# Performance work log

Hardware: AMD Instinct MI355X
Metric: run time of the kernel (lower is better)

Reference implementation:

```python
import jax, jax.numpy as jnp
import numpy as np

N_NODES = 100000
N_EDGES = 1600000
IN_FEATS = 256
OUT_FEATS = 64


def setup_inputs() -> dict:
    key = jax.random.key(0)
    k1, k2, k3, k4, k5, k6 = jax.random.split(key, 6)
    x = jax.random.normal(k1, (N_NODES, IN_FEATS), dtype=jnp.float32)
    edge_src = jax.random.randint(k2, (N_EDGES,), 0, N_NODES, dtype=jnp.int32)
    edge_dst = jax.random.randint(k3, (N_EDGES,), 0, N_NODES, dtype=jnp.int32)
    edge_weight = jax.random.uniform(k4, (N_EDGES,), dtype=jnp.float32)
    # Linear(in_feats, out_feats) params (Kaiming-uniform-ish init scale)
    scale = 1.0 / np.sqrt(IN_FEATS)
    W = jax.random.uniform(k5, (IN_FEATS, OUT_FEATS), minval=-scale, maxval=scale, dtype=jnp.float32)
    b = jax.random.uniform(k6, (OUT_FEATS,), minval=-scale, maxval=scale, dtype=jnp.float32)
    return {"x": x, "edge_src": edge_src, "edge_dst": edge_dst,
            "edge_weight": edge_weight, "W": W, "b": b}


def reference(x, edge_src, edge_dst, edge_weight, W, b):
    # h = fc(x)
    h = x @ W + b                                   # [N, out_feats]
    # spmm(graph, h): out[dst] += w * h[src]  (weighted adjacency matvec)
    msgs = h[edge_src] * edge_weight[:, None]       # [E, out_feats]
    out = jax.ops.segment_sum(msgs, edge_dst, num_segments=N_NODES)
    return out
```

## Files before the change

kernel.cpp:

```cpp
#include <hip/hip_runtime.h>

#define IN_F 256
#define OUT_F 64
#define SORT_CHUNK 4096
#define BKT_SHIFT 7
#define BKT_NODES 128
#define MAX_NB 1024

typedef __attribute__((ext_vector_type(8))) short short8;
typedef __attribute__((ext_vector_type(4))) float f32x4;

static __device__ __forceinline__ short f2bf(float f) {
    union { float f; unsigned u; } v; v.f = f;
    unsigned r = v.u + 0x7FFFu + ((v.u >> 16) & 1u);
    return (short)(r >> 16);
}
static __device__ __forceinline__ float bf2f(short s) {
    return __int_as_float(((unsigned)(unsigned short)s) << 16);
}

__global__ __launch_bounds__(256)
void prep_w_kernel(const float* __restrict__ W, short* __restrict__ Wt) {
    int i = blockIdx.x * 256 + threadIdx.x;
    if (i < IN_F * OUT_F) {
        int k = i / OUT_F, n = i % OUT_F;
        Wt[n * IN_F + k] = f2bf(W[i]);
    }
}

__global__ __launch_bounds__(256, 4)
void fc_bhist_kernel(const float* __restrict__ x, const short* __restrict__ Wt,
                     const float* __restrict__ bias, short* __restrict__ h,
                     const int* __restrict__ dst, int* __restrict__ counts,
                     int nRows, int nE, int NB, int nSB, int nHist) {
    __shared__ __align__(16) char smem[OUT_F * IN_F * sizeof(short)];
    if ((int)blockIdx.x < nHist) {
        int* lh = (int*)smem;
        const int cb = blockIdx.x;
        for (int b0 = threadIdx.x; b0 < NB; b0 += 256) lh[b0] = 0;
        __syncthreads();
        const int base = cb * SORT_CHUNK;
        const int lim = min(nE, base + SORT_CHUNK);
        const int4* d4 = (const int4*)(dst + base);
        const int n4 = (lim - base) >> 2;
        for (int i = threadIdx.x; i < n4; i += 256) {
            int4 v = d4[i];
            atomicAdd(&lh[v.x >> BKT_SHIFT], 1);
            atomicAdd(&lh[v.y >> BKT_SHIFT], 1);
            atomicAdd(&lh[v.z >> BKT_SHIFT], 1);
            atomicAdd(&lh[v.w >> BKT_SHIFT], 1);
        }
        for (int e = base + (n4 << 2) + threadIdx.x; e < lim; e += 256)
            atomicAdd(&lh[dst[e] >> BKT_SHIFT], 1);
        __syncthreads();
        for (int b0 = threadIdx.x; b0 < NB; b0 += 256)
            counts[b0 * nSB + cb] = lh[b0];
        return;
    }
    short* Wl = (short*)smem;
    {
        const uint4* src = (const uint4*)Wt;
        #pragma unroll
        for (int it = 0; it < 8; ++it) {
            int g = it * 256 + threadIdx.x;
            int n = g >> 5, s = g & 31;
            *(uint4*)((char*)Wl + n * 512 + (s ^ (n & 7)) * 16) = src[g];
        }
    }
    __syncthreads();

    const int wv = threadIdx.x >> 6;
    const int l  = threadIdx.x & 63;
    const int lr = l & 15;
    const int kg = l >> 4;

    const int fb = blockIdx.x - nHist;
    const int rowbase = (fb * 4 + wv) * 32;
    if (rowbase >= nRows) return;

    const int ar0 = min(rowbase + lr,      nRows - 1);
    const int ar1 = min(rowbase + 16 + lr, nRows - 1);
    const float* xp0 = x + (size_t)ar0 * IN_F + kg * 8;
    const float* xp1 = x + (size_t)ar1 * IN_F + kg * 8;

    f32x4 acc[2][4];
    #pragma unroll
    for (int m = 0; m < 2; ++m)
        #pragma unroll
        for (int n = 0; n < 4; ++n) acc[m][n] = (f32x4)0.f;

    #pragma unroll
    for (int kt = 0; kt < 8; ++kt) {
        const int K0 = kt * 32;
        float4 a0lo = *(const float4*)(xp0 + K0);
        float4 a0hi = *(const float4*)(xp0 + K0 + 4);
        float4 a1lo = *(const float4*)(xp1 + K0);
        float4 a1hi = *(const float4*)(xp1 + K0 + 4);

        short8 a0, a1;
        a0[0] = f2bf(a0lo.x); a0[1] = f2bf(a0lo.y);
        a0[2] = f2bf(a0lo.z); a0[3] = f2bf(a0lo.w);
        a0[4] = f2bf(a0hi.x); a0[5] = f2bf(a0hi.y);
        a0[6] = f2bf(a0hi.z); a0[7] = f2bf(a0hi.w);
        a1[0] = f2bf(a1lo.x); a1[1] = f2bf(a1lo.y);
        a1[2] = f2bf(a1lo.z); a1[3] = f2bf(a1lo.w);
        a1[4] = f2bf(a1hi.x); a1[5] = f2bf(a1hi.y);
        a1[6] = f2bf(a1hi.z); a1[7] = f2bf(a1hi.w);

        short8 bf[4];
        #pragma unroll
        for (int nt = 0; nt < 4; ++nt) {
            const int col = nt * 16 + lr;
            const int slot = (kt * 4 + kg) ^ (col & 7);
            bf[nt] = *(const short8*)((const char*)Wl + col * 512 + slot * 16);
        }
        #pragma unroll
        for (int nt = 0; nt < 4; ++nt) {
            acc[0][nt] = __builtin_amdgcn_mfma_f32_16x16x32_bf16(a0, bf[nt], acc[0][nt], 0, 0, 0);
            acc[1][nt] = __builtin_amdgcn_mfma_f32_16x16x32_bf16(a1, bf[nt], acc[1][nt], 0, 0, 0);
        }
    }

    #pragma unroll
    for (int m = 0; m < 2; ++m) {
        #pragma unroll
        for (int nt = 0; nt < 4; ++nt) {
            const int col = nt * 16 + lr;
            const float bb = bias[col];
            #pragma unroll
            for (int j = 0; j < 4; ++j) {
                const int r = rowbase + m * 16 + kg * 4 + j;
                if (r < nRows)
                    h[(size_t)r * OUT_F + col] = f2bf(acc[m][nt][j] + bb);
            }
        }
    }
}

__global__ __launch_bounds__(256)
void scan1_kernel(const int* __restrict__ cnt, int* __restrict__ off,
                  int* __restrict__ part, int n) {
    __shared__ int sh[256];
    int base = blockIdx.x * 1024;
    int t = threadIdx.x;
    int v[4]; int s = 0;
    #pragma unroll
    for (int i = 0; i < 4; ++i) {
        int idx = base + t * 4 + i;
        v[i] = (idx < n) ? cnt[idx] : 0;
        s += v[i];
    }
    sh[t] = s;
    __syncthreads();
    for (int d = 1; d < 256; d <<= 1) {
        int val = (t >= d) ? sh[t - d] : 0;
        __syncthreads();
        sh[t] += val;
        __syncthreads();
    }
    if (t == 255) part[blockIdx.x] = sh[255];
    int run = (t == 0) ? 0 : sh[t - 1];
    #pragma unroll
    for (int i = 0; i < 4; ++i) {
        int idx = base + t * 4 + i;
        if (idx < n) off[idx] = run;
        run += v[i];
    }
}

__global__ __launch_bounds__(256)
void scan2_kernel(int* __restrict__ part, int nPart) {
    __shared__ int sh[256];
    int t = threadIdx.x;
    int v[4]; int s = 0;
    #pragma unroll
    for (int i = 0; i < 4; ++i) {
        int idx = t * 4 + i;
        v[i] = (idx < nPart) ? part[idx] : 0;
        s += v[i];
    }
    sh[t] = s;
    __syncthreads();
    for (int d = 1; d < 256; d <<= 1) {
        int val = (t >= d) ? sh[t - d] : 0;
        __syncthreads();
        sh[t] += val;
        __syncthreads();
    }
    int run = (t == 0) ? 0 : sh[t - 1];
    #pragma unroll
    for (int i = 0; i < 4; ++i) {
        int idx = t * 4 + i;
        if (idx < nPart) part[idx] = run;
        run += v[i];
    }
}

__global__ __launch_bounds__(256)
void bfill_kernel(const int* __restrict__ src, const int* __restrict__ dst,
                  const float* __restrict__ w, const int* __restrict__ bases,
                  const int* __restrict__ part, int2* __restrict__ pack,
                  int nE, int NB, int nSB) {
    __shared__ int cur[MAX_NB];
    const int cb = blockIdx.x;
    for (int b0 = threadIdx.x; b0 < NB; b0 += 256) {
        int idx = b0 * nSB + cb;
        cur[b0] = bases[idx] + part[idx >> 10];
    }
    __syncthreads();
    const int base = cb * SORT_CHUNK;
    const int lim = min(nE, base + SORT_CHUNK);
    const int4* s4 = (const int4*)(src + base);
    const int4* d4 = (const int4*)(dst + base);
    const float4* w4 = (const float4*)(w + base);
    const int n4 = (lim - base) >> 2;
    for (int i = threadIdx.x; i < n4; i += 256) {
        int4 s = s4[i]; int4 d = d4[i]; float4 ww = w4[i];
        int p0 = atomicAdd(&cur[d.x >> BKT_SHIFT], 1);
        pack[p0] = make_int2(s.x | ((d.x & (BKT_NODES - 1)) << 17), __float_as_int(ww.x));
        int p1 = atomicAdd(&cur[d.y >> BKT_SHIFT], 1);
        pack[p1] = make_int2(s.y | ((d.y & (BKT_NODES - 1)) << 17), __float_as_int(ww.y));
        int p2 = atomicAdd(&cur[d.z >> BKT_SHIFT], 1);
        pack[p2] = make_int2(s.z | ((d.z & (BKT_NODES - 1)) << 17), __float_as_int(ww.z));
        int p3 = atomicAdd(&cur[d.w >> BKT_SHIFT], 1);
        pack[p3] = make_int2(s.w | ((d.w & (BKT_NODES - 1)) << 17), __float_as_int(ww.w));
    }
    for (int e = base + (n4 << 2) + threadIdx.x; e < lim; e += 256) {
        int d = dst[e];
        int p = atomicAdd(&cur[d >> BKT_SHIFT], 1);
        pack[p] = make_int2(src[e] | ((d & (BKT_NODES - 1)) << 17),
                            __float_as_int(w[e]));
    }
}

__global__ __launch_bounds__(256)
void nsort_kernel(const int2* __restrict__ pack, const int* __restrict__ bases,
                  const int* __restrict__ part, int2* __restrict__ pack2,
                  int* __restrict__ off, int nRows, int nE, int NB, int nSB) {
    __shared__ int cnt[BKT_NODES];
    __shared__ int scn[BKT_NODES];
    const int b = blockIdx.x;
    const int tid = threadIdx.x;
    const int i0 = b * nSB;
    const int segStart = bases[i0] + part[i0 >> 10];
    int segEnd = nE;
    if (b + 1 < NB) {
        int i1 = (b + 1) * nSB;
        segEnd = bases[i1] + part[i1 >> 10];
    }

    if (tid < BKT_NODES) cnt[tid] = 0;
    __syncthreads();
    {
        int e = segStart + tid;
        for (; e + 768 < segEnd; e += 1024) {
            int a0 = pack[e].x, a1 = pack[e + 256].x;
            int a2 = pack[e + 512].x, a3 = pack[e + 768].x;
            atomicAdd(&cnt[(a0 >> 17) & (BKT_NODES - 1)], 1);
            atomicAdd(&cnt[(a1 >> 17) & (BKT_NODES - 1)], 1);
            atomicAdd(&cnt[(a2 >> 17) & (BKT_NODES - 1)], 1);
            atomicAdd(&cnt[(a3 >> 17) & (BKT_NODES - 1)], 1);
        }
        for (; e < segEnd; e += 256)
            atomicAdd(&cnt[(pack[e].x >> 17) & (BKT_NODES - 1)], 1);
    }
    __syncthreads();

    if (tid < BKT_NODES) scn[tid] = cnt[tid];
    __syncthreads();
    for (int d = 1; d < BKT_NODES; d <<= 1) {
        int t = 0;
        if (tid < BKT_NODES && tid >= d) t = scn[tid - d];
        __syncthreads();
        if (tid < BKT_NODES) scn[tid] += t;
        __syncthreads();
    }

    const int node0 = b * BKT_NODES;
    const int ncnt = min(BKT_NODES, nRows - node0);
    if (tid < ncnt)
        off[node0 + tid] = segStart + scn[tid] - cnt[tid];
    if (tid == 0 && node0 + ncnt == nRows)
        off[nRows] = segEnd;
    __syncthreads();

    if (tid < BKT_NODES) cnt[tid] = segStart + scn[tid] - cnt[tid];
    __syncthreads();
    {
        int e = segStart + tid;
        for (; e + 768 < segEnd; e += 1024) {
            int2 p0 = pack[e], p1 = pack[e + 256];
            int2 p2 = pack[e + 512], p3 = pack[e + 768];
            int q0 = atomicAdd(&cnt[(p0.x >> 17) & (BKT_NODES - 1)], 1);
            pack2[q0] = make_int2(p0.x & 0x1FFFF, p0.y);
            int q1 = atomicAdd(&cnt[(p1.x >> 17) & (BKT_NODES - 1)], 1);
            pack2[q1] = make_int2(p1.x & 0x1FFFF, p1.y);
            int q2 = atomicAdd(&cnt[(p2.x >> 17) & (BKT_NODES - 1)], 1);
            pack2[q2] = make_int2(p2.x & 0x1FFFF, p2.y);
            int q3 = atomicAdd(&cnt[(p3.x >> 17) & (BKT_NODES - 1)], 1);
            pack2[q3] = make_int2(p3.x & 0x1FFFF, p3.y);
        }
        for (; e < segEnd; e += 256) {
            int2 p = pack[e];
            int q = atomicAdd(&cnt[(p.x >> 17) & (BKT_NODES - 1)], 1);
            pack2[q] = make_int2(p.x & 0x1FFFF, p.y);
        }
    }
}

__global__ __launch_bounds__(256)
void ngather_kernel(const short* __restrict__ h, const int* __restrict__ off,
                    const int2* __restrict__ pack2, float* __restrict__ out,
                    int nNodes) {
    int wid = (blockIdx.x * 256 + threadIdx.x) >> 6;
    int lane = threadIdx.x & 63;
    if (wid >= nNodes) return;
    int e = off[wid], end = off[wid + 1];
    const ushort* hu = (const ushort*)h;
    float acc = 0.f;
    for (; e + 8 <= end; e += 8) {
        int2 pk[8];
        #pragma unroll
        for (int i = 0; i < 8; ++i) pk[i] = pack2[e + i];
        float hv[8];
        #pragma unroll
        for (int i = 0; i < 8; ++i)
            hv[i] = bf2f((short)hu[(size_t)pk[i].x * OUT_F + lane]);
        #pragma unroll
        for (int i = 0; i < 8; ++i)
            acc = fmaf(__int_as_float(pk[i].y), hv[i], acc);
    }
    for (; e + 4 <= end; e += 4) {
        int2 pk[4];
        #pragma unroll
        for (int i = 0; i < 4; ++i) pk[i] = pack2[e + i];
        #pragma unroll
        for (int i = 0; i < 4; ++i)
            acc = fmaf(__int_as_float(pk[i].y),
                       bf2f((short)hu[(size_t)pk[i].x * OUT_F + lane]), acc);
    }
    for (; e < end; ++e) {
        int2 p = pack2[e];
        acc = fmaf(__int_as_float(p.y),
                   bf2f((short)hu[(size_t)p.x * OUT_F + lane]), acc);
    }
    out[(size_t)wid * OUT_F + lane] = acc;
}

__global__ __launch_bounds__(256)
void scatter_kernel(const short* __restrict__ h, const int* __restrict__ src,
                    const int* __restrict__ dst, const float* __restrict__ w,
                    float* __restrict__ out, int nE) {
    int t = blockIdx.x * 256 + threadIdx.x;
    int c = t & 15;
    int stride = (gridDim.x * 256) >> 4;
    for (int e = t >> 4; e < nE; e += stride) {
        int s = src[e];
        int d = dst[e];
        float ww = w[e];
        float* op = out + (size_t)d * OUT_F + c * 4;
        const short* hp = h + (size_t)s * OUT_F + c * 4;
        unsafeAtomicAdd(op + 0, ww * bf2f(hp[0]));
        unsafeAtomicAdd(op + 1, ww * bf2f(hp[1]));
        unsafeAtomicAdd(op + 2, ww * bf2f(hp[2]));
        unsafeAtomicAdd(op + 3, ww * bf2f(hp[3]));
    }
}

static inline size_t align256(size_t x) { return (x + 255) & ~(size_t)255; }

extern "C" void kernel_launch(void* const* d_in, const int* in_sizes, int n_in,
                              void* d_out, int out_size, void* d_ws, size_t ws_size,
                              hipStream_t stream) {
    const float* x    = (const float*)d_in[0];
    const int*   esrc = (const int*)d_in[1];
    const int*   edst = (const int*)d_in[2];
    const float* ew   = (const float*)d_in[3];
    const float* W    = (const float*)d_in[4];
    const float* b    = (const float*)d_in[5];

    int nRows = in_sizes[0] / IN_F;
    int nE    = in_sizes[1];

    int NB  = (nRows + BKT_NODES - 1) / BKT_NODES;
    int nSB = (nE + SORT_CHUNK - 1) / SORT_CHUNK;
    int nCnt = NB * nSB;
    int nPart = (nCnt + 1023) / 1024;

    char* p = (char*)d_ws;
    size_t hB    = align256((size_t)nRows * OUT_F * sizeof(short));
    size_t wtB   = align256((size_t)IN_F * OUT_F * sizeof(short));
    size_t cntB  = align256((size_t)nCnt * sizeof(int));
    size_t basB  = align256((size_t)nCnt * sizeof(int));
    size_t partB = align256((size_t)nPart * sizeof(int));
    size_t packB = align256((size_t)nE * sizeof(int2));
    size_t offB  = align256((size_t)(nRows + 1) * sizeof(int));
    size_t need  = hB + wtB + cntB + basB + partB + 2 * packB + offB;

    short* h      = (short*)p;  p += hB;
    short* Wt     = (short*)p;  p += wtB;
    int*   counts = (int*)p;    p += cntB;
    int*   bases  = (int*)p;    p += basB;
    int*   part   = (int*)p;    p += partB;
    int2*  pack   = (int2*)p;   p += packB;
    int2*  pack2  = (int2*)p;   p += packB;
    int*   off    = (int*)p;

    float* out = (float*)d_out;

    bool ok = (ws_size >= need) && (NB <= MAX_NB) && (nPart <= 1024) &&
              (nRows < (1 << 17));
    int nHist = ok ? nSB : 0;
    int fcBlocks = (nRows + 127) / 128;

    prep_w_kernel<<<(IN_F * OUT_F + 255) / 256, 256, 0, stream>>>(W, Wt);
    fc_bhist_kernel<<<nHist + fcBlocks, 256, 0, stream>>>(
        x, Wt, b, h, edst, counts, nRows, nE, NB, nSB, nHist);

    if (ok) {
        scan1_kernel<<<nPart, 256, 0, stream>>>(counts, bases, part, nCnt);
        scan2_kernel<<<1, 256, 0, stream>>>(part, nPart);
        bfill_kernel<<<nSB, 256, 0, stream>>>(esrc, edst, ew, bases, part,
                                              pack, nE, NB, nSB);
        nsort_kernel<<<NB, 256, 0, stream>>>(pack, bases, part, pack2, off,
                                             nRows, nE, NB, nSB);
        int gBlocks = (nRows * 64 + 255) / 256;
        ngather_kernel<<<gBlocks, 256, 0, stream>>>(h, off, pack2, out, nRows);
    } else {
        hipMemsetAsync(out, 0, (size_t)out_size * sizeof(float), stream);
        scatter_kernel<<<4096, 256, 0, stream>>>(h, esrc, edst, ew, out, nE);
    }
}
```

Measured before the change: 286.4 us.

## Fuse FC, bucket sort and gather into one cooperative persistent kernel

Replaces the chain of separate launches (weight prep, fc+histogram, two scans, bucket fill, node sort, gather) with a single cooperative kernel. The phases are separated by grid.sync and run in persistent grid-stride loops. Weight bf16 conversion and swizzling now happen inside each block instead of in a separate prep kernel. This removes launch gaps and tail effects between phases. In exchange the grid is capped at occupancy-limited size (at most 1024 blocks), which may reduce parallelism in the gather and GEMM phases, and it adds grid-wide barrier costs plus host-side occupancy queries on every call.

```diff
diff --git a/kernel.cpp b/kernel.cpp
--- a/kernel.cpp
+++ b/kernel.cpp
@@ -1,4 +1,7 @@
 #include <hip/hip_runtime.h>
+#include <hip/hip_cooperative_groups.h>
+
+namespace cg = cooperative_groups;
 
 #define IN_F 256
 #define OUT_F 64
@@ -6,6 +9,7 @@
 #define BKT_SHIFT 7
 #define BKT_NODES 128
 #define MAX_NB 1024
+#define GRID_MAX 1024
 
 typedef __attribute__((ext_vector_type(8))) short short8;
 typedef __attribute__((ext_vector_type(4))) float f32x4;
@@ -19,67 +23,35 @@
     return __int_as_float(((unsigned)(unsigned short)s) << 16);
 }
 
-__global__ __launch_bounds__(256)
-void prep_w_kernel(const float* __restrict__ W, short* __restrict__ Wt) {
-    int i = blockIdx.x * 256 + threadIdx.x;
-    if (i < IN_F * OUT_F) {
-        int k = i / OUT_F, n = i % OUT_F;
-        Wt[n * IN_F + k] = f2bf(W[i]);
-    }
-}
-
-__global__ __launch_bounds__(256, 4)
-void fc_bhist_kernel(const float* __restrict__ x, const short* __restrict__ Wt,
-                     const float* __restrict__ bias, short* __restrict__ h,
-                     const int* __restrict__ dst, int* __restrict__ counts,
-                     int nRows, int nE, int NB, int nSB, int nHist) {
-    __shared__ __align__(16) char smem[OUT_F * IN_F * sizeof(short)];
-    if ((int)blockIdx.x < nHist) {
-        int* lh = (int*)smem;
-        const int cb = blockIdx.x;
-        for (int b0 = threadIdx.x; b0 < NB; b0 += 256) lh[b0] = 0;
-        __syncthreads();
-        const int base = cb * SORT_CHUNK;
-        const int lim = min(nE, base + SORT_CHUNK);
-        const int4* d4 = (const int4*)(dst + base);
-        const int n4 = (lim - base) >> 2;
-        for (int i = threadIdx.x; i < n4; i += 256) {
-            int4 v = d4[i];
-            atomicAdd(&lh[v.x >> BKT_SHIFT], 1);
-            atomicAdd(&lh[v.y >> BKT_SHIFT], 1);
-            atomicAdd(&lh[v.z >> BKT_SHIFT], 1);
-            atomicAdd(&lh[v.w >> BKT_SHIFT], 1);
-        }
-        for (int e = base + (n4 << 2) + threadIdx.x; e < lim; e += 256)
-            atomicAdd(&lh[dst[e] >> BKT_SHIFT], 1);
-        __syncthreads();
-        for (int b0 = threadIdx.x; b0 < NB; b0 += 256)
-            counts[b0 * nSB + cb] = lh[b0];
-        return;
-    }
-    short* Wl = (short*)smem;
-    {
-        const uint4* src = (const uint4*)Wt;
-        #pragma unroll
-        for (int it = 0; it < 8; ++it) {
-            int g = it * 256 + threadIdx.x;
-            int n = g >> 5, s = g & 31;
-            *(uint4*)((char*)Wl + n * 512 + (s ^ (n & 7)) * 16) = src[g];
-        }
-    }
-    __syncthreads();
-
-    const int wv = threadIdx.x >> 6;
-    const int l  = threadIdx.x & 63;
+
+static __device__ __forceinline__ void stage_W(const float* __restrict__ W,
+                                               short* Wl, int tid) {
+    const int n0 = tid & 63;
+    const int kb = tid >> 6;
+    #pragma unroll
+    for (int K0 = 0; K0 < 64; K0 += 8) {
+        const int k0 = kb * 64 + K0;
+        short8 v;
+        #pragma unroll
+        for (int j = 0; j < 8; ++j)
+            v[j] = f2bf(W[(k0 + j) * OUT_F + n0]);
+        *(short8*)((char*)Wl + n0 * 512 + (((k0 >> 3)) ^ (n0 & 7)) * 16) = v;
+    }
+}
+
+static __device__ __forceinline__ void gemm_tile(const float* __restrict__ x,
+                                                 const short* Wl,
+                                                 const float* __restrict__ bias,
+                                                 short* __restrict__ h,
+                                                 int rowbase, int nRows, int tid) {
+    const int wv = tid >> 6;
+    const int l  = tid & 63;
     const int lr = l & 15;
     const int kg = l >> 4;
-
-    const int fb = blockIdx.x - nHist;
-    const int rowbase = (fb * 4 + wv) * 32;
-    if (rowbase >= nRows) return;
-
-    const int ar0 = min(rowbase + lr,      nRows - 1);
-    const int ar1 = min(rowbase + 16 + lr, nRows - 1);
+    const int rb = rowbase + wv * 32;
+    if (rb >= nRows) return;
+    const int ar0 = min(rb + lr,      nRows - 1);
+    const int ar1 = min(rb + 16 + lr, nRows - 1);
     const float* xp0 = x + (size_t)ar0 * IN_F + kg * 8;
     const float* xp1 = x + (size_t)ar1 * IN_F + kg * 8;
 
@@ -129,7 +101,7 @@
             const float bb = bias[col];
             #pragma unroll
             for (int j = 0; j < 4; ++j) {
-                const int r = rowbase + m * 16 + kg * 4 + j;
+                const int r = rb + m * 16 + kg * 4 + j;
                 if (r < nRows)
                     h[(size_t)r * OUT_F + col] = f2bf(acc[m][nt][j] + bb);
             }
@@ -137,73 +109,37 @@
     }
 }
 
-__global__ __launch_bounds__(256)
-void scan1_kernel(const int* __restrict__ cnt, int* __restrict__ off,
-                  int* __restrict__ part, int n) {
-    __shared__ int sh[256];
-    int base = blockIdx.x * 1024;
-    int t = threadIdx.x;
-    int v[4]; int s = 0;
-    #pragma unroll
-    for (int i = 0; i < 4; ++i) {
-        int idx = base + t * 4 + i;
-        v[i] = (idx < n) ? cnt[idx] : 0;
-        s += v[i];
-    }
-    sh[t] = s;
-    __syncthreads();
-    for (int d = 1; d < 256; d <<= 1) {
-        int val = (t >= d) ? sh[t - d] : 0;
-        __syncthreads();
-        sh[t] += val;
-        __syncthreads();
-    }
-    if (t == 255) part[blockIdx.x] = sh[255];
-    int run = (t == 0) ? 0 : sh[t - 1];
-    #pragma unroll
-    for (int i = 0; i < 4; ++i) {
-        int idx = base + t * 4 + i;
-        if (idx < n) off[idx] = run;
-        run += v[i];
-    }
-}
-
-__global__ __launch_bounds__(256)
-void scan2_kernel(int* __restrict__ part, int nPart) {
-    __shared__ int sh[256];
-    int t = threadIdx.x;
-    int v[4]; int s = 0;
-    #pragma unroll
-    for (int i = 0; i < 4; ++i) {
-        int idx = t * 4 + i;
-        v[i] = (idx < nPart) ? part[idx] : 0;
-        s += v[i];
-    }
-    sh[t] = s;
-    __syncthreads();
-    for (int d = 1; d < 256; d <<= 1) {
-        int val = (t >= d) ? sh[t - d] : 0;
-        __syncthreads();
-        sh[t] += val;
-        __syncthreads();
-    }
-    int run = (t == 0) ? 0 : sh[t - 1];
-    #pragma unroll
-    for (int i = 0; i < 4; ++i) {
-        int idx = t * 4 + i;
-        if (idx < nPart) part[idx] = run;
-        run += v[i];
-    }
-}
-
-__global__ __launch_bounds__(256)
-void bfill_kernel(const int* __restrict__ src, const int* __restrict__ dst,
-                  const float* __restrict__ w, const int* __restrict__ bases,
-                  const int* __restrict__ part, int2* __restrict__ pack,
-                  int nE, int NB, int nSB) {
-    __shared__ int cur[MAX_NB];
-    const int cb = blockIdx.x;
-    for (int b0 = threadIdx.x; b0 < NB; b0 += 256) {
+static __device__ __forceinline__ void hist_chunk(const int* __restrict__ dst,
+                                                  int* lh, int* __restrict__ counts,
+                                                  int cb, int nE, int NB, int nSB,
+                                                  int tid) {
+    for (int b0 = tid; b0 < NB; b0 += 256) lh[b0] = 0;
+    __syncthreads();
+    const int base = cb * SORT_CHUNK;
+    const int lim = min(nE, base + SORT_CHUNK);
+    const int4* d4 = (const int4*)(dst + base);
+    const int n4 = (lim - base) >> 2;
+    for (int i = tid; i < n4; i += 256) {
+        int4 v = d4[i];
+        atomicAdd(&lh[v.x >> BKT_SHIFT], 1);
+        atomicAdd(&lh[v.y >> BKT_SHIFT], 1);
+        atomicAdd(&lh[v.z >> BKT_SHIFT], 1);
+        atomicAdd(&lh[v.w >> BKT_SHIFT], 1);
+    }
+    for (int e = base + (n4 << 2) + tid; e < lim; e += 256)
+        atomicAdd(&lh[dst[e] >> BKT_SHIFT], 1);
+    __syncthreads();
+    for (int b0 = tid; b0 < NB; b0 += 256)
+        counts[b0 * nSB + cb] = lh[b0];
+    __syncthreads();
+}
+
+static __device__ __forceinline__ void bfill_chunk(
+        const int* __restrict__ src, const int* __restrict__ dst,
+        const float* __restrict__ w, const int* __restrict__ bases,
+        const int* __restrict__ part, int2* __restrict__ pack,
+        int* cur, int cb, int nE, int NB, int nSB, int tid) {
+    for (int b0 = tid; b0 < NB; b0 += 256) {
         int idx = b0 * nSB + cb;
         cur[b0] = bases[idx] + part[idx >> 10];
     }
@@ -214,7 +150,7 @@
     const int4* d4 = (const int4*)(dst + base);
     const float4* w4 = (const float4*)(w + base);
     const int n4 = (lim - base) >> 2;
-    for (int i = threadIdx.x; i < n4; i += 256) {
+    for (int i = tid; i < n4; i += 256) {
         int4 s = s4[i]; int4 d = d4[i]; float4 ww = w4[i];
         int p0 = atomicAdd(&cur[d.x >> BKT_SHIFT], 1);
         pack[p0] = make_int2(s.x | ((d.x & (BKT_NODES - 1)) << 17), __float_as_int(ww.x));
@@ -225,22 +161,20 @@
         int p3 = atomicAdd(&cur[d.w >> BKT_SHIFT], 1);
         pack[p3] = make_int2(s.w | ((d.w & (BKT_NODES - 1)) << 17), __float_as_int(ww.w));
     }
-    for (int e = base + (n4 << 2) + threadIdx.x; e < lim; e += 256) {
+    for (int e = base + (n4 << 2) + tid; e < lim; e += 256) {
         int d = dst[e];
         int p = atomicAdd(&cur[d >> BKT_SHIFT], 1);
         pack[p] = make_int2(src[e] | ((d & (BKT_NODES - 1)) << 17),
                             __float_as_int(w[e]));
     }
-}
-
-__global__ __launch_bounds__(256)
-void nsort_kernel(const int2* __restrict__ pack, const int* __restrict__ bases,
-                  const int* __restrict__ part, int2* __restrict__ pack2,
-                  int* __restrict__ off, int nRows, int nE, int NB, int nSB) {
-    __shared__ int cnt[BKT_NODES];
-    __shared__ int scn[BKT_NODES];
-    const int b = blockIdx.x;
-    const int tid = threadIdx.x;
+    __syncthreads();
+}
+
+static __device__ __forceinline__ void nsort_bucket(
+        const int2* __restrict__ pack, const int* __restrict__ bases,
+        const int* __restrict__ part, int2* __restrict__ pack2,
+        int* __restrict__ off, int* cnt, int* scn,
+        int b, int nRows, int nE, int NB, int nSB, int tid) {
     const int i0 = b * nSB;
     const int segStart = bases[i0] + part[i0 >> 10];
     int segEnd = nE;
@@ -248,7 +182,6 @@
         int i1 = (b + 1) * nSB;
         segEnd = bases[i1] + part[i1 >> 10];
     }
-
     if (tid < BKT_NODES) cnt[tid] = 0;
     __syncthreads();
     {
@@ -265,7 +198,6 @@
             atomicAdd(&cnt[(pack[e].x >> 17) & (BKT_NODES - 1)], 1);
     }
     __syncthreads();
-
     if (tid < BKT_NODES) scn[tid] = cnt[tid];
     __syncthreads();
     for (int d = 1; d < BKT_NODES; d <<= 1) {
@@ -275,7 +207,6 @@
         if (tid < BKT_NODES) scn[tid] += t;
         __syncthreads();
     }
-
     const int node0 = b * BKT_NODES;
     const int ncnt = min(BKT_NODES, nRows - node0);
     if (tid < ncnt)
@@ -283,7 +214,6 @@
     if (tid == 0 && node0 + ncnt == nRows)
         off[nRows] = segEnd;
     __syncthreads();
-
     if (tid < BKT_NODES) cnt[tid] = segStart + scn[tid] - cnt[tid];
     __syncthreads();
     {
@@ -306,6 +236,248 @@
             pack2[q] = make_int2(p.x & 0x1FFFF, p.y);
         }
     }
+    __syncthreads();
+}
+
+static __device__ __forceinline__ float gather_node(
+        const ushort* __restrict__ hu, const int2* __restrict__ pack2,
+        int e, int end, int lane) {
+    float acc = 0.f;
+    for (; e + 8 <= end; e += 8) {
+        int2 pk[8];
+        #pragma unroll
+        for (int i = 0; i < 8; ++i) pk[i] = pack2[e + i];
+        float hv[8];
+        #pragma unroll
+        for (int i = 0; i < 8; ++i)
+            hv[i] = bf2f((short)hu[(size_t)pk[i].x * OUT_F + lane]);
+        #pragma unroll
+        for (int i = 0; i < 8; ++i)
+            acc = fmaf(__int_as_float(pk[i].y), hv[i], acc);
+    }
+    for (; e + 4 <= end; e += 4) {
+        int2 pk[4];
+        #pragma unroll
+        for (int i = 0; i < 4; ++i) pk[i] = pack2[e + i];
+        #pragma unroll
+        for (int i = 0; i < 4; ++i)
+            acc = fmaf(__int_as_float(pk[i].y),
+                       bf2f((short)hu[(size_t)pk[i].x * OUT_F + lane]), acc);
+    }
+    for (; e < end; ++e) {
+        int2 p = pack2[e];
+        acc = fmaf(__int_as_float(p.y),
+                   bf2f((short)hu[(size_t)p.x * OUT_F + lane]), acc);
+    }
+    return acc;
+}
+
+__global__ __launch_bounds__(256, 4)
+void mega_kernel(const float* __restrict__ x, const int* __restrict__ esrc,
+                 const int* __restrict__ edst, const float* __restrict__ ew,
+                 const float* __restrict__ W, const float* __restrict__ bias,
+                 short* __restrict__ h, int* __restrict__ counts,
+                 int* __restrict__ bases, int* __restrict__ part,
+                 int2* __restrict__ pack, int2* __restrict__ pack2,
+                 int* __restrict__ off, float* __restrict__ out,
+                 int nRows, int nE, int NB, int nSB, int nCnt, int nPart) {
+    cg::grid_group grid = cg::this_grid();
+    __shared__ __align__(16) char smem[32768];
+    const int tid = threadIdx.x;
+    const int bid = blockIdx.x;
+    const int nBlk = gridDim.x;
+
+    for (int cb = bid; cb < nSB; cb += nBlk)
+        hist_chunk(edst, (int*)smem, counts, cb, nE, NB, nSB, tid);
+
+    {
+        const int nTiles = (nRows + 127) / 128;
+        if (bid < nTiles) {
+            short* Wl = (short*)smem;
+            stage_W(W, Wl, tid);
+            __syncthreads();
+            for (int t = bid; t < nTiles; t += nBlk)
+                gemm_tile(x, Wl, bias, h, t * 128, nRows, tid);
+        }
+    }
+    grid.sync();
+
+    {
+        int* sh = (int*)smem;
+        for (int s = bid; s < nPart; s += nBlk) {
+            const int base = s * 1024;
+            int v[4]; int sum = 0;
+            #pragma unroll
+            for (int i = 0; i < 4; ++i) {
+                int idx = base + tid * 4 + i;
+                v[i] = (idx < nCnt) ? counts[idx] : 0;
+                sum += v[i];
+            }
+            sh[tid] = sum;
+            __syncthreads();
+            for (int d = 1; d < 256; d <<= 1) {
+                int val = (tid >= d) ? sh[tid - d] : 0;
+                __syncthreads();
+                sh[tid] += val;
+                __syncthreads();
+            }
+            if (tid == 255) part[s] = sh[255];
+            int run = (tid == 0) ? 0 : sh[tid - 1];
+            #pragma unroll
+            for (int i = 0; i < 4; ++i) {
+                int idx = base + tid * 4 + i;
+                if (idx < nCnt) bases[idx] = run;
+                run += v[i];
+            }
+            __syncthreads();
+        }
+    }
+    grid.sync();
+
+    if (bid == 0) {
+        int* sh = (int*)smem;
+        int v[4]; int sum = 0;
+        #pragma unroll
+        for (int i = 0; i < 4; ++i) {
+            int idx = tid * 4 + i;
+            v[i] = (idx < nPart) ? part[idx] : 0;
+            sum += v[i];
+        }
+        sh[tid] = sum;
+        __syncthreads();
+        for (int d = 1; d < 256; d <<= 1) {
+            int val = (tid >= d) ? sh[tid - d] : 0;
+            __syncthreads();
+            sh[tid] += val;
+            __syncthreads();
+        }
+        int run = (tid == 0) ? 0 : sh[tid - 1];
+        #pragma unroll
+        for (int i = 0; i < 4; ++i) {
+            int idx = tid * 4 + i;
+            if (idx < nPart) part[idx] = run;
+            run += v[i];
+        }
+    }
+    grid.sync();
+
+    for (int cb = bid; cb < nSB; cb += nBlk)
+        bfill_chunk(esrc, edst, ew, bases, part, pack, (int*)smem,
+                    cb, nE, NB, nSB, tid);
+    grid.sync();
+
+    {
+        int* cnt = (int*)smem;
+        int* scn = cnt + BKT_NODES;
+        for (int b = bid; b < NB; b += nBlk)
+            nsort_bucket(pack, bases, part, pack2, off, cnt, scn,
+                         b, nRows, nE, NB, nSB, tid);
+    }
+    grid.sync();
+
+    {
+        const int lane = tid & 63;
+        const int nW = (nBlk * 256) >> 6;
+        const ushort* hu = (const ushort*)h;
+        for (int wid = (bid * 256 + tid) >> 6; wid < nRows; wid += nW)
+            out[(size_t)wid * OUT_F + lane] =
+                gather_node(hu, pack2, off[wid], off[wid + 1], lane);
+    }
+}
+
+__global__ __launch_bounds__(256, 4)
+void fc_bhist_kernel(const float* __restrict__ x, const float* __restrict__ W,
+                     const float* __restrict__ bias, short* __restrict__ h,
+                     const int* __restrict__ dst, int* __restrict__ counts,
+                     int nRows, int nE, int NB, int nSB, int nHist) {
+    __shared__ __align__(16) char smem[32768];
+    if ((int)blockIdx.x < nHist) {
+        hist_chunk(dst, (int*)smem, counts, blockIdx.x, nE, NB, nSB, threadIdx.x);
+        return;
+    }
+    short* Wl = (short*)smem;
+    stage_W(W, Wl, threadIdx.x);
+    __syncthreads();
+    gemm_tile(x, Wl, bias, h, (blockIdx.x - nHist) * 128, nRows, threadIdx.x);
+}
+
+__global__ __launch_bounds__(256)
+void scan1_kernel(const int* __restrict__ cnt, int* __restrict__ off,
+                  int* __restrict__ part, int n) {
+    __shared__ int sh[256];
+    int base = blockIdx.x * 1024;
+    int t = threadIdx.x;
+    int v[4]; int s = 0;
+    #pragma unroll
+    for (int i = 0; i < 4; ++i) {
+        int idx = base + t * 4 + i;
+        v[i] = (idx < n) ? cnt[idx] : 0;
+        s += v[i];
+    }
+    sh[t] = s;
+    __syncthreads();
+    for (int d = 1; d < 256; d <<= 1) {
+        int val = (t >= d) ? sh[t - d] : 0;
+        __syncthreads();
+        sh[t] += val;
+        __syncthreads();
+    }
+    if (t == 255) part[blockIdx.x] = sh[255];
+    int run = (t == 0) ? 0 : sh[t - 1];
+    #pragma unroll
+    for (int i = 0; i < 4; ++i) {
+        int idx = base + t * 4 + i;
+        if (idx < n) off[idx] = run;
+        run += v[i];
+    }
+}
+
+__global__ __launch_bounds__(256)
+void scan2_kernel(int* __restrict__ part, int nPart) {
+    __shared__ int sh[256];
+    int t = threadIdx.x;
+    int v[4]; int s = 0;
+    #pragma unroll
+    for (int i = 0; i < 4; ++i) {
+        int idx = t * 4 + i;
+        v[i] = (idx < nPart) ? part[idx] : 0;
+        s += v[i];
+    }
+    sh[t] = s;
+    __syncthreads();
+    for (int d = 1; d < 256; d <<= 1) {
+        int val = (t >= d) ? sh[t - d] : 0;
+        __syncthreads();
+        sh[t] += val;
+        __syncthreads();
+    }
+    int run = (t == 0) ? 0 : sh[t - 1];
+    #pragma unroll
+    for (int i = 0; i < 4; ++i) {
+        int idx = t * 4 + i;
+        if (idx < nPart) part[idx] = run;
+        run += v[i];
+    }
+}
+
+__global__ __launch_bounds__(256)
+void bfill_kernel(const int* __restrict__ src, const int* __restrict__ dst,
+                  const float* __restrict__ w, const int* __restrict__ bases,
+                  const int* __restrict__ part, int2* __restrict__ pack,
+                  int nE, int NB, int nSB) {
+    __shared__ int cur[MAX_NB];
+    bfill_chunk(src, dst, w, bases, part, pack, cur,
+                blockIdx.x, nE, NB, nSB, threadIdx.x);
+}
+
+__global__ __launch_bounds__(256)
+void nsort_kernel(const int2* __restrict__ pack, const int* __restrict__ bases,
+                  const int* __restrict__ part, int2* __restrict__ pack2,
+                  int* __restrict__ off, int nRows, int nE, int NB, int nSB) {
+    __shared__ int cnt[BKT_NODES];
+    __shared__ int scn[BKT_NODES];
+    nsort_bucket(pack, bases, part, pack2, off, cnt, scn,
+                 blockIdx.x, nRows, nE, NB, nSB, threadIdx.x);
 }
 
 __global__ __launch_bounds__(256)
@@ -315,36 +487,8 @@
     int wid = (blockIdx.x * 256 + threadIdx.x) >> 6;
     int lane = threadIdx.x & 63;
     if (wid >= nNodes) return;
-    int e = off[wid], end = off[wid + 1];
-    const ushort* hu = (const ushort*)h;
-    float acc = 0.f;
-    for (; e + 8 <= end; e += 8) {
-        int2 pk[8];
-        #pragma unroll
-        for (int i = 0; i < 8; ++i) pk[i] = pack2[e + i];
-        float hv[8];
-        #pragma unroll
-        for (int i = 0; i < 8; ++i)
-            hv[i] = bf2f((short)hu[(size_t)pk[i].x * OUT_F + lane]);
-        #pragma unroll
-        for (int i = 0; i < 8; ++i)
-            acc = fmaf(__int_as_float(pk[i].y), hv[i], acc);
-    }
-    for (; e + 4 <= end; e += 4) {
-        int2 pk[4];
-        #pragma unroll
-        for (int i = 0; i < 4; ++i) pk[i] = pack2[e + i];
-        #pragma unroll
-        for (int i = 0; i < 4; ++i)
-            acc = fmaf(__int_as_float(pk[i].y),
-                       bf2f((short)hu[(size_t)pk[i].x * OUT_F + lane]), acc);
-    }
-    for (; e < end; ++e) {
-        int2 p = pack2[e];
-        acc = fmaf(__int_as_float(p.y),
-                   bf2f((short)hu[(size_t)p.x * OUT_F + lane]), acc);
-    }
-    out[(size_t)wid * OUT_F + lane] = acc;
+    out[(size_t)wid * OUT_F + lane] =
+        gather_node((const ushort*)h, pack2, off[wid], off[wid + 1], lane);
 }
 
 __global__ __launch_bounds__(256)
@@ -389,16 +533,14 @@
 
     char* p = (char*)d_ws;
     size_t hB    = align256((size_t)nRows * OUT_F * sizeof(short));
-    size_t wtB   = align256((size_t)IN_F * OUT_F * sizeof(short));
     size_t cntB  = align256((size_t)nCnt * sizeof(int));
     size_t basB  = align256((size_t)nCnt * sizeof(int));
     size_t partB = align256((size_t)nPart * sizeof(int));
     size_t packB = align256((size_t)nE * sizeof(int2));
     size_t offB  = align256((size_t)(nRows + 1) * sizeof(int));
-    size_t need  = hB + wtB + cntB + basB + partB + 2 * packB + offB;
+    size_t need  = hB + cntB + basB + partB + 2 * packB + offB;
 
     short* h      = (short*)p;  p += hB;
-    short* Wt     = (short*)p;  p += wtB;
     int*   counts = (int*)p;    p += cntB;
     int*   bases  = (int*)p;    p += basB;
     int*   part   = (int*)p;    p += partB;
@@ -410,24 +552,49 @@
 
     bool ok = (ws_size >= need) && (NB <= MAX_NB) && (nPart <= 1024) &&
               (nRows < (1 << 17));
-    int nHist = ok ? nSB : 0;
-    int fcBlocks = (nRows + 127) / 128;
-
-    prep_w_kernel<<<(IN_F * OUT_F + 255) / 256, 256, 0, stream>>>(W, Wt);
-    fc_bhist_kernel<<<nHist + fcBlocks, 256, 0, stream>>>(
-        x, Wt, b, h, edst, counts, nRows, nE, NB, nSB, nHist);
-
-    if (ok) {
-        scan1_kernel<<<nPart, 256, 0, stream>>>(counts, bases, part, nCnt);
-        scan2_kernel<<<1, 256, 0, stream>>>(part, nPart);
-        bfill_kernel<<<nSB, 256, 0, stream>>>(esrc, edst, ew, bases, part,
-                                              pack, nE, NB, nSB);
-        nsort_kernel<<<NB, 256, 0, stream>>>(pack, bases, part, pack2, off,
-                                             nRows, nE, NB, nSB);
-        int gBlocks = (nRows * 64 + 255) / 256;
-        ngather_kernel<<<gBlocks, 256, 0, stream>>>(h, off, pack2, out, nRows);
-    } else {
+    if (!ok) {
+        int fcBlocks = (nRows + 127) / 128;
+        fc_bhist_kernel<<<fcBlocks, 256, 0, stream>>>(
+            x, W, b, h, edst, counts, nRows, nE, NB, nSB, 0);
         hipMemsetAsync(out, 0, (size_t)out_size * sizeof(float), stream);
         scatter_kernel<<<4096, 256, 0, stream>>>(h, esrc, edst, ew, out, nE);
-    }
-}
+        return;
+    }
+
+    int dev = 0, numCU = 0, maxBpc = 0;
+    hipGetDevice(&dev);
+    hipDeviceGetAttribute(&numCU, hipDeviceAttributeMultiprocessorCount, dev);
+    hipError_t occErr = hipOccupancyMaxActiveBlocksPerMultiprocessor(
+        &maxBpc, (const void*)mega_kernel, 256, 0);
+    int grid = 0;
+    if (occErr == hipSuccess && maxBpc > 0 && numCU > 0)
+        grid = min(GRID_MAX, maxBpc * numCU);
+
+    hipError_t launchErr = hipErrorUnknown;
+    if (grid >= 64) {
+        void* kargs[] = {
+            (void*)&x, (void*)&esrc, (void*)&edst, (void*)&ew,
+            (void*)&W, (void*)&b,
+            (void*)&h, (void*)&counts, (void*)&bases, (void*)&part,
+            (void*)&pack, (void*)&pack2, (void*)&off, (void*)&out,
+            (void*)&nRows, (void*)&nE, (void*)&NB, (void*)&nSB,
+            (void*)&nCnt, (void*)&nPart
+        };
+        launchErr = hipLaunchCooperativeKernel((const void*)mega_kernel,
+                                               dim3(grid), dim3(256),
+                                               kargs, 0, stream);
+    }
+    if (launchErr == hipSuccess) return;
+
+    int fcBlocks = (nRows + 127) / 128;
+    fc_bhist_kernel<<<nSB + fcBlocks, 256, 0, stream>>>(
+        x, W, b, h, edst, counts, nRows, nE, NB, nSB, nSB);
+    scan1_kernel<<<nPart, 256, 0, stream>>>(counts, bases, part, nCnt);
+    scan2_kernel<<<1, 256, 0, stream>>>(part, nPart);
+    bfill_kernel<<<nSB, 256, 0, stream>>>(esrc, edst, ew, bases, part,
+                                          pack, nE, NB, nSB);
+    nsort_kernel<<<NB, 256, 0, stream>>>(pack, bases, part, pack2, off,
+                                         nRows, nE, NB, nSB);
+    int gBlocks = (nRows * 64 + 255) / 256;
+    ngather_kernel<<<gBlocks, 256, 0, stream>>>(h, off, pack2, out, nRows);
+}
```

Result: slower. 690.0 us (+140.9%).

## Fold weight prep into GEMM blocks and part-scan into bfill/nsort

Applied to the files above, without the earlier changes.

Removes the separate prep_w kernel by having each GEMM block convert and transpose W from fp32 into swizzled bf16 shared memory directly. It also drops the single-block scan2 kernel, with each bfill and nsort block redundantly scanning the partition totals in shared memory. The aim is to cut two kernel launches and their serialization gaps. The cost is redundant work per block: strided uncoalesced W reads across ~782 GEMM blocks, and a 256-thread scan repeated in every bfill and nsort block.

```diff
diff --git a/kernel.cpp b/kernel.cpp
--- a/kernel.cpp
+++ b/kernel.cpp
@@ -19,67 +19,35 @@
     return __int_as_float(((unsigned)(unsigned short)s) << 16);
 }
 
-__global__ __launch_bounds__(256)
-void prep_w_kernel(const float* __restrict__ W, short* __restrict__ Wt) {
-    int i = blockIdx.x * 256 + threadIdx.x;
-    if (i < IN_F * OUT_F) {
-        int k = i / OUT_F, n = i % OUT_F;
-        Wt[n * IN_F + k] = f2bf(W[i]);
-    }
-}
-
-__global__ __launch_bounds__(256, 4)
-void fc_bhist_kernel(const float* __restrict__ x, const short* __restrict__ Wt,
-                     const float* __restrict__ bias, short* __restrict__ h,
-                     const int* __restrict__ dst, int* __restrict__ counts,
-                     int nRows, int nE, int NB, int nSB, int nHist) {
-    __shared__ __align__(16) char smem[OUT_F * IN_F * sizeof(short)];
-    if ((int)blockIdx.x < nHist) {
-        int* lh = (int*)smem;
-        const int cb = blockIdx.x;
-        for (int b0 = threadIdx.x; b0 < NB; b0 += 256) lh[b0] = 0;
-        __syncthreads();
-        const int base = cb * SORT_CHUNK;
-        const int lim = min(nE, base + SORT_CHUNK);
-        const int4* d4 = (const int4*)(dst + base);
-        const int n4 = (lim - base) >> 2;
-        for (int i = threadIdx.x; i < n4; i += 256) {
-            int4 v = d4[i];
-            atomicAdd(&lh[v.x >> BKT_SHIFT], 1);
-            atomicAdd(&lh[v.y >> BKT_SHIFT], 1);
-            atomicAdd(&lh[v.z >> BKT_SHIFT], 1);
-            atomicAdd(&lh[v.w >> BKT_SHIFT], 1);
-        }
-        for (int e = base + (n4 << 2) + threadIdx.x; e < lim; e += 256)
-            atomicAdd(&lh[dst[e] >> BKT_SHIFT], 1);
-        __syncthreads();
-        for (int b0 = threadIdx.x; b0 < NB; b0 += 256)
-            counts[b0 * nSB + cb] = lh[b0];
-        return;
-    }
-    short* Wl = (short*)smem;
-    {
-        const uint4* src = (const uint4*)Wt;
-        #pragma unroll
-        for (int it = 0; it < 8; ++it) {
-            int g = it * 256 + threadIdx.x;
-            int n = g >> 5, s = g & 31;
-            *(uint4*)((char*)Wl + n * 512 + (s ^ (n & 7)) * 16) = src[g];
-        }
-    }
-    __syncthreads();
-
-    const int wv = threadIdx.x >> 6;
-    const int l  = threadIdx.x & 63;
+
+static __device__ __forceinline__ void stage_W(const float* __restrict__ W,
+                                               short* Wl, int tid) {
+    const int n0 = tid & 63;
+    const int kb = tid >> 6;
+    #pragma unroll
+    for (int K0 = 0; K0 < 64; K0 += 8) {
+        const int k0 = kb * 64 + K0;
+        short8 v;
+        #pragma unroll
+        for (int j = 0; j < 8; ++j)
+            v[j] = f2bf(W[(k0 + j) * OUT_F + n0]);
+        *(short8*)((char*)Wl + n0 * 512 + (((k0 >> 3)) ^ (n0 & 7)) * 16) = v;
+    }
+}
+
+static __device__ __forceinline__ void gemm_tile(const float* __restrict__ x,
+                                                 const short* Wl,
+                                                 const float* __restrict__ bias,
+                                                 short* __restrict__ h,
+                                                 int rowbase, int nRows, int tid) {
+    const int wv = tid >> 6;
+    const int l  = tid & 63;
     const int lr = l & 15;
     const int kg = l >> 4;
-
-    const int fb = blockIdx.x - nHist;
-    const int rowbase = (fb * 4 + wv) * 32;
-    if (rowbase >= nRows) return;
-
-    const int ar0 = min(rowbase + lr,      nRows - 1);
-    const int ar1 = min(rowbase + 16 + lr, nRows - 1);
+    const int rb = rowbase + wv * 32;
+    if (rb >= nRows) return;
+    const int ar0 = min(rb + lr,      nRows - 1);
+    const int ar1 = min(rb + 16 + lr, nRows - 1);
     const float* xp0 = x + (size_t)ar0 * IN_F + kg * 8;
     const float* xp1 = x + (size_t)ar1 * IN_F + kg * 8;
 
@@ -129,12 +97,80 @@
             const float bb = bias[col];
             #pragma unroll
             for (int j = 0; j < 4; ++j) {
-                const int r = rowbase + m * 16 + kg * 4 + j;
+                const int r = rb + m * 16 + kg * 4 + j;
                 if (r < nRows)
                     h[(size_t)r * OUT_F + col] = f2bf(acc[m][nt][j] + bb);
             }
         }
     }
+}
+
+static __device__ __forceinline__ void hist_chunk(const int* __restrict__ dst,
+                                                  int* lh, int* __restrict__ counts,
+                                                  int cb, int nE, int NB, int nSB,
+                                                  int tid) {
+    for (int b0 = tid; b0 < NB; b0 += 256) lh[b0] = 0;
+    __syncthreads();
+    const int base = cb * SORT_CHUNK;
+    const int lim = min(nE, base + SORT_CHUNK);
+    const int4* d4 = (const int4*)(dst + base);
+    const int n4 = (lim - base) >> 2;
+    for (int i = tid; i < n4; i += 256) {
+        int4 v = d4[i];
+        atomicAdd(&lh[v.x >> BKT_SHIFT], 1);
+        atomicAdd(&lh[v.y >> BKT_SHIFT], 1);
+        atomicAdd(&lh[v.z >> BKT_SHIFT], 1);
+        atomicAdd(&lh[v.w >> BKT_SHIFT], 1);
+    }
+    for (int e = base + (n4 << 2) + tid; e < lim; e += 256)
+        atomicAdd(&lh[dst[e] >> BKT_SHIFT], 1);
+    __syncthreads();
+    for (int b0 = tid; b0 < NB; b0 += 256)
+        counts[b0 * nSB + cb] = lh[b0];
+    __syncthreads();
+}
+
+static __device__ __forceinline__ void local_part_scan(
+        const int* __restrict__ part, int nPart, int* partS, int* sh, int tid) {
+    int v[4]; int sum = 0;
+    #pragma unroll
+    for (int i = 0; i < 4; ++i) {
+        int idx = tid * 4 + i;
+        v[i] = (idx < nPart) ? part[idx] : 0;
+        sum += v[i];
+    }
+    sh[tid] = sum;
+    __syncthreads();
+    for (int d = 1; d < 256; d <<= 1) {
+        int val = (tid >= d) ? sh[tid - d] : 0;
+        __syncthreads();
+        sh[tid] += val;
+        __syncthreads();
+    }
+    int run = (tid == 0) ? 0 : sh[tid - 1];
+    #pragma unroll
+    for (int i = 0; i < 4; ++i) {
+        partS[tid * 4 + i] = run;
+        run += v[i];
+    }
+    __syncthreads();
+}
+
+
+__global__ __launch_bounds__(256, 4)
+void fc_bhist_kernel(const float* __restrict__ x, const float* __restrict__ W,
+                     const float* __restrict__ bias, short* __restrict__ h,
+                     const int* __restrict__ dst, int* __restrict__ counts,
+                     int nRows, int nE, int NB, int nSB, int nHist) {
+    __shared__ __align__(16) char smem[32768];
+    if ((int)blockIdx.x < nHist) {
+        hist_chunk(dst, (int*)smem, counts, blockIdx.x, nE, NB, nSB, threadIdx.x);
+        return;
+    }
+    short* Wl = (short*)smem;
+    stage_W(W, Wl, threadIdx.x);
+    __syncthreads();
+    gemm_tile(x, Wl, bias, h, (blockIdx.x - nHist) * 128, nRows, threadIdx.x);
 }
 
 __global__ __launch_bounds__(256)
@@ -169,43 +205,19 @@
 }
 
 __global__ __launch_bounds__(256)
-void scan2_kernel(int* __restrict__ part, int nPart) {
-    __shared__ int sh[256];
-    int t = threadIdx.x;
-    int v[4]; int s = 0;
-    #pragma unroll
-    for (int i = 0; i < 4; ++i) {
-        int idx = t * 4 + i;
-        v[i] = (idx < nPart) ? part[idx] : 0;
-        s += v[i];
-    }
-    sh[t] = s;
-    __syncthreads();
-    for (int d = 1; d < 256; d <<= 1) {
-        int val = (t >= d) ? sh[t - d] : 0;
-        __syncthreads();
-        sh[t] += val;
-        __syncthreads();
-    }
-    int run = (t == 0) ? 0 : sh[t - 1];
-    #pragma unroll
-    for (int i = 0; i < 4; ++i) {
-        int idx = t * 4 + i;
-        if (idx < nPart) part[idx] = run;
-        run += v[i];
-    }
-}
-
-__global__ __launch_bounds__(256)
 void bfill_kernel(const int* __restrict__ src, const int* __restrict__ dst,
                   const float* __restrict__ w, const int* __restrict__ bases,
                   const int* __restrict__ part, int2* __restrict__ pack,
-                  int nE, int NB, int nSB) {
+                  int nE, int NB, int nSB, int nPart) {
     __shared__ int cur[MAX_NB];
+    __shared__ int partS[MAX_NB];
+    __shared__ int sh[256];
+    const int tid = threadIdx.x;
     const int cb = blockIdx.x;
-    for (int b0 = threadIdx.x; b0 < NB; b0 += 256) {
+    local_part_scan(part, nPart, partS, sh, tid);
+    for (int b0 = tid; b0 < NB; b0 += 256) {
         int idx = b0 * nSB + cb;
-        cur[b0] = bases[idx] + part[idx >> 10];
+        cur[b0] = bases[idx] + partS[idx >> 10];
     }
     __syncthreads();
     const int base = cb * SORT_CHUNK;
@@ -214,7 +226,7 @@
     const int4* d4 = (const int4*)(dst + base);
     const float4* w4 = (const float4*)(w + base);
     const int n4 = (lim - base) >> 2;
-    for (int i = threadIdx.x; i < n4; i += 256) {
+    for (int i = tid; i < n4; i += 256) {
         int4 s = s4[i]; int4 d = d4[i]; float4 ww = w4[i];
         int p0 = atomicAdd(&cur[d.x >> BKT_SHIFT], 1);
         pack[p0] = make_int2(s.x | ((d.x & (BKT_NODES - 1)) << 17), __float_as_int(ww.x));
@@ -225,7 +237,7 @@
         int p3 = atomicAdd(&cur[d.w >> BKT_SHIFT], 1);
         pack[p3] = make_int2(s.w | ((d.w & (BKT_NODES - 1)) << 17), __float_as_int(ww.w));
     }
-    for (int e = base + (n4 << 2) + threadIdx.x; e < lim; e += 256) {
+    for (int e = base + (n4 << 2) + tid; e < lim; e += 256) {
         int d = dst[e];
         int p = atomicAdd(&cur[d >> BKT_SHIFT], 1);
         pack[p] = make_int2(src[e] | ((d & (BKT_NODES - 1)) << 17),
@@ -236,19 +248,23 @@
 __global__ __launch_bounds__(256)
 void nsort_kernel(const int2* __restrict__ pack, const int* __restrict__ bases,
                   const int* __restrict__ part, int2* __restrict__ pack2,
-                  int* __restrict__ off, int nRows, int nE, int NB, int nSB) {
+                  int* __restrict__ off, int nRows, int nE, int NB, int nSB,
+                  int nPart) {
     __shared__ int cnt[BKT_NODES];
     __shared__ int scn[BKT_NODES];
+    __shared__ int partS[MAX_NB];
+    __shared__ int sh[256];
     const int b = blockIdx.x;
     const int tid = threadIdx.x;
+    local_part_scan(part, nPart, partS, sh, tid);
+
     const int i0 = b * nSB;
-    const int segStart = bases[i0] + part[i0 >> 10];
+    const int segStart = bases[i0] + partS[i0 >> 10];
     int segEnd = nE;
     if (b + 1 < NB) {
         int i1 = (b + 1) * nSB;
-        segEnd = bases[i1] + part[i1 >> 10];
-    }
-
+        segEnd = bases[i1] + partS[i1 >> 10];
+    }
     if (tid < BKT_NODES) cnt[tid] = 0;
     __syncthreads();
     {
@@ -265,7 +281,6 @@
             atomicAdd(&cnt[(pack[e].x >> 17) & (BKT_NODES - 1)], 1);
     }
     __syncthreads();
-
     if (tid < BKT_NODES) scn[tid] = cnt[tid];
     __syncthreads();
     for (int d = 1; d < BKT_NODES; d <<= 1) {
@@ -275,7 +290,6 @@
         if (tid < BKT_NODES) scn[tid] += t;
         __syncthreads();
     }
-
     const int node0 = b * BKT_NODES;
     const int ncnt = min(BKT_NODES, nRows - node0);
     if (tid < ncnt)
@@ -283,7 +297,6 @@
     if (tid == 0 && node0 + ncnt == nRows)
         off[nRows] = segEnd;
     __syncthreads();
-
     if (tid < BKT_NODES) cnt[tid] = segStart + scn[tid] - cnt[tid];
     __syncthreads();
     {
@@ -389,16 +402,14 @@
 
     char* p = (char*)d_ws;
     size_t hB    = align256((size_t)nRows * OUT_F * sizeof(short));
-    size_t wtB   = align256((size_t)IN_F * OUT_F * sizeof(short));
     size_t cntB  = align256((size_t)nCnt * sizeof(int));
     size_t basB  = align256((size_t)nCnt * sizeof(int));
     size_t partB = align256((size_t)nPart * sizeof(int));
     size_t packB = align256((size_t)nE * sizeof(int2));
     size_t offB  = align256((size_t)(nRows + 1) * sizeof(int));
-    size_t need  = hB + wtB + cntB + basB + partB + 2 * packB + offB;
+    size_t need  = hB + cntB + basB + partB + 2 * packB + offB;
 
     short* h      = (short*)p;  p += hB;
-    short* Wt     = (short*)p;  p += wtB;
     int*   counts = (int*)p;    p += cntB;
     int*   bases  = (int*)p;    p += basB;
     int*   part   = (int*)p;    p += partB;
@@ -410,24 +421,23 @@
 
     bool ok = (ws_size >= need) && (NB <= MAX_NB) && (nPart <= 1024) &&
               (nRows < (1 << 17));
-    int nHist = ok ? nSB : 0;
     int fcBlocks = (nRows + 127) / 128;
 
-    prep_w_kernel<<<(IN_F * OUT_F + 255) / 256, 256, 0, stream>>>(W, Wt);
-    fc_bhist_kernel<<<nHist + fcBlocks, 256, 0, stream>>>(
-        x, Wt, b, h, edst, counts, nRows, nE, NB, nSB, nHist);
-
-    if (ok) {
-        scan1_kernel<<<nPart, 256, 0, stream>>>(counts, bases, part, nCnt);
-        scan2_kernel<<<1, 256, 0, stream>>>(part, nPart);
-        bfill_kernel<<<nSB, 256, 0, stream>>>(esrc, edst, ew, bases, part,
-                                              pack, nE, NB, nSB);
-        nsort_kernel<<<NB, 256, 0, stream>>>(pack, bases, part, pack2, off,
-                                             nRows, nE, NB, nSB);
-        int gBlocks = (nRows * 64 + 255) / 256;
-        ngather_kernel<<<gBlocks, 256, 0, stream>>>(h, off, pack2, out, nRows);
-    } else {
+    if (!ok) {
+        fc_bhist_kernel<<<fcBlocks, 256, 0, stream>>>(
+            x, W, b, h, edst, counts, nRows, nE, NB, nSB, 0);
         hipMemsetAsync(out, 0, (size_t)out_size * sizeof(float), stream);
         scatter_kernel<<<4096, 256, 0, stream>>>(h, esrc, edst, ew, out, nE);
-    }
-}
+        return;
+    }
+
+    fc_bhist_kernel<<<nSB + fcBlocks, 256, 0, stream>>>(
+        x, W, b, h, edst, counts, nRows, nE, NB, nSB, nSB);
+    scan1_kernel<<<nPart, 256, 0, stream>>>(counts, bases, part, nCnt);
+    bfill_kernel<<<nSB, 256, 0, stream>>>(esrc, edst, ew, bases, part,
+                                          pack, nE, NB, nSB, nPart);
+    nsort_kernel<<<NB, 256, 0, stream>>>(pack, bases, part, pack2, off,
+                                         nRows, nE, NB, nSB, nPart);
+    int gBlocks = (nRows * 64 + 255) / 256;
+    ngather_kernel<<<gBlocks, 256, 0, stream>>>(h, off, pack2, out, nRows);
+}
```

Measured after the change: 284.7 us. Within noise of the previous version (-0.6%).
